# Kernel optimization log

Measured on AMD Instinct MI355X. Metric: run time of the kernel, lower is better.

## Reference

```python
import jax, jax.numpy as jnp
import numpy as np

T, HID, D, NQ, NKV = 4096, 2048, 128, 16, 4
THETA = 10000.0


def _rope(x, pos):
    # x: [T, N, D], non-interleaved (rotate_half) RoPE
    half = D // 2
    inv_freq = 1.0 / (THETA ** (jnp.arange(0, half, dtype=jnp.float32) / half))
    freqs = pos.astype(jnp.float32)[:, None] * inv_freq[None, :]  # [T, half]
    cos = jnp.cos(freqs)[:, None, :]  # [T, 1, half]
    sin = jnp.sin(freqs)[:, None, :]
    x1, x2 = x[..., :half], x[..., half:]
    return jnp.concatenate([x1 * cos - x2 * sin, x2 * cos + x1 * sin], axis=-1)


def setup_inputs() -> dict:
    key = jax.random.key(0)
    ks = jax.random.split(key, 5)
    s = 0.02
    return {
        "hidden_states": jax.random.normal(ks[0], (T, HID), jnp.float32),
        "wq": jax.random.normal(ks[1], (HID, HID), jnp.float32) * s,
        "wk": jax.random.normal(ks[2], (NKV * D, HID), jnp.float32) * s,
        "wv": jax.random.normal(ks[3], (NKV * D, HID), jnp.float32) * s,
        "wo": jax.random.normal(ks[4], (HID, HID), jnp.float32) * s,
        "position_ids": jnp.arange(T, dtype=jnp.int32),
    }


def reference(hidden_states, wq, wk, wv, wo, position_ids):
    q = (hidden_states @ wq.T).reshape(T, NQ, D)
    k = (hidden_states @ wk.T).reshape(T, NKV, D)
    v = (hidden_states @ wv.T).reshape(T, NKV, D)
    q = _rope(q, position_ids)
    k = _rope(k, position_ids)
    # GQA: share each KV head across NQ//NKV query heads
    rep = NQ // NKV
    k = jnp.repeat(k, rep, axis=1)  # [T, NQ, D]
    v = jnp.repeat(v, rep, axis=1)
    scale = 1.0 / jnp.sqrt(jnp.float32(D))
    scores = jnp.einsum("qhd,khd->hqk", q, k) * scale  # [NQ, T, T]
    causal = jnp.tril(jnp.ones((T, T), dtype=bool))
    scores = jnp.where(causal[None, :, :], scores, jnp.float32(-1e30))
    probs = jax.nn.softmax(scores, axis=-1)
    out = jnp.einsum("hqk,khd->qhd", probs, v).reshape(T, HID)
    return out @ wo.T
```

## Files before the change

kernel.cpp:

```cpp
#include <hip/hip_runtime.h>
#include <hip/hip_bf16.h>
#include <cstdint>

#define T_    4096
#define HID_  2048
#define DH    128
#define NQ_   16
#define NKV_  4
#define QKVW  3072

typedef __attribute__((ext_vector_type(8))) short bf16x8;
typedef __attribute__((ext_vector_type(4))) float f32x4;
typedef __attribute__((ext_vector_type(16))) float f32x16;
typedef __attribute__((ext_vector_type(4))) float f4;
typedef __attribute__((ext_vector_type(4))) short s4;

__device__ __forceinline__ short f2bf(float f) {
  union { float f; unsigned u; } x; x.f = f;
  unsigned r = x.u + 0x7fffu + ((x.u >> 16) & 1u);
  return (short)(r >> 16);
}
__device__ __forceinline__ float bf2f(short s) {
  return __uint_as_float(((unsigned)(unsigned short)s) << 16);
}
__device__ __forceinline__ unsigned pkbf2(float a, float b) {
  union { __hip_bfloat162 h; unsigned u; } c;
  c.h = __float22bfloat162_rn(make_float2(a, b));
  return c.u;
}

__device__ __forceinline__ void gload16(const void* g, void* l) {
  __builtin_amdgcn_global_load_lds(
      (const __attribute__((address_space(1))) unsigned*)g,
      (__attribute__((address_space(3))) unsigned*)l, 16, 0, 0);
}

#define MFMA16(a, b, c) __builtin_amdgcn_mfma_f32_16x16x32_bf16(a, b, c, 0, 0, 0)
#define MFMA32(a, b, c) __builtin_amdgcn_mfma_f32_32x32x16_bf16(a, b, c, 0, 0, 0)

#define Z16 {0.f,0.f,0.f,0.f,0.f,0.f,0.f,0.f,0.f,0.f,0.f,0.f,0.f,0.f,0.f,0.f}
#define SCL2 0.127517432f

#define C_HS 2097152u
#define C_WQ (C_HS + 1048576u)
#define C_WK (C_WQ + 262144u)
#define C_WV (C_WK + 262144u)
#define C_WO (C_WV + 1048576u)
__global__ void cvt_all(const float* __restrict__ hs, const float* __restrict__ wq,
                        const float* __restrict__ wk, const float* __restrict__ wv,
                        const float* __restrict__ wo, short* __restrict__ hs_bf,
                        short* __restrict__ w1_bf, short* __restrict__ wo_bf) {
  const unsigned stride = gridDim.x * blockDim.x;
  for (unsigned i = blockIdx.x * blockDim.x + threadIdx.x; i < C_WO; i += stride) {
    const float* s; short* d; unsigned off;
    if (i < C_HS)      { s = hs; d = hs_bf;           off = i; }
    else if (i < C_WQ) { s = wq; d = w1_bf;           off = i - C_HS; }
    else if (i < C_WK) { s = wk; d = w1_bf + 4194304; off = i - C_WQ; }
    else if (i < C_WV) { s = wv; d = w1_bf + 5242880; off = i - C_WK; }
    else               { s = wo; d = wo_bf;           off = i - C_WV; }
    f4 v = ((const f4*)s)[off];
    s4 o;
    o[0] = f2bf(v[0]); o[1] = f2bf(v[1]); o[2] = f2bf(v[2]); o[3] = f2bf(v[3]);
    ((s4*)d)[off] = o;
  }
}

template <int BF16OUT>
__global__ __launch_bounds__(256) void gemm_bt(const short* __restrict__ A,
                                               const short* __restrict__ B,
                                               void* __restrict__ Cp,
                                               int N, int K) {
  __shared__ short lA[128 * 32];
  __shared__ short lB[128 * 32];
  const int nb = gridDim.x * gridDim.y;
  const int lin = blockIdx.y * gridDim.x + blockIdx.x;
  const int per = nb >> 3;
  const int wg = (lin & 7) * per + (lin >> 3);
  const int bx = wg % gridDim.x;
  const int by = wg / gridDim.x;

  const int tid = threadIdx.x;
  const int lane = tid & 63;
  const int w = tid >> 6;
  const int wr = w >> 1, wc = w & 1;
  const int l15 = lane & 15, l4 = lane >> 4;
  f32x4 acc[4][4];
#pragma unroll
  for (int m = 0; m < 4; m++)
#pragma unroll
    for (int n = 0; n < 4; n++) acc[m][n] = f32x4{0.f, 0.f, 0.f, 0.f};

  const short* Ag = A + (size_t)bx * 128 * K;
  const short* Bg = B + (size_t)by * 128 * K;

  for (int kt = 0; kt < K; kt += 32) {
#pragma unroll
    for (int i = 0; i < 2; ++i) {
      const int cb = i * 256 + w * 64;
      const int c = cb + lane;
      const int row = c >> 2, eo = (c & 3) << 3;
      gload16(Ag + (size_t)row * K + kt + eo, &lA[cb * 8]);
      gload16(Bg + (size_t)row * K + kt + eo, &lB[cb * 8]);
    }
    __syncthreads();
    bf16x8 af[4], bfr[4];
#pragma unroll
    for (int m = 0; m < 4; m++)
      af[m] = *(const bf16x8*)&lA[(wr * 64 + m * 16 + l15) * 32 + l4 * 8];
#pragma unroll
    for (int n = 0; n < 4; n++)
      bfr[n] = *(const bf16x8*)&lB[(wc * 64 + n * 16 + l15) * 32 + l4 * 8];
#pragma unroll
    for (int m = 0; m < 4; m++)
#pragma unroll
      for (int n = 0; n < 4; n++)
        acc[m][n] = MFMA16(af[m], bfr[n], acc[m][n]);
    __syncthreads();
  }

  const int r0 = bx * 128 + wr * 64;
  const int c0 = by * 128 + wc * 64;
#pragma unroll
  for (int m = 0; m < 4; m++)
#pragma unroll
    for (int n = 0; n < 4; n++)
#pragma unroll
      for (int r = 0; r < 4; r++) {
        const int row = r0 + m * 16 + l4 * 4 + r;
        const int col = c0 + n * 16 + l15;
        if (BF16OUT)
          ((short*)Cp)[(size_t)row * N + col] = f2bf(acc[m][n][r]);
        else
          ((float*)Cp)[(size_t)row * N + col] = acc[m][n][r];
      }
}

__global__ void rope_k(short* __restrict__ qkv, const int* __restrict__ pos) {
  const int row = blockIdx.x;
  const int sub = threadIdx.x >> 6;
  const int d = threadIdx.x & 63;
  const int head = blockIdx.y * 4 + sub;
  const int col0 = (head < NQ_) ? head * DH : HID_ + (head - NQ_) * DH;
  const float scl = (head < NQ_) ? SCL2 : 1.0f;
  short* p = qkv + (size_t)row * QKVW + col0;
  const float fp = (float)pos[row];
  const float freq = fp * powf(10000.0f, -(float)d * (1.0f / 64.0f));
  const float sn = sinf(freq), cs = cosf(freq);
  const float x1 = bf2f(p[d]);
  const float x2 = bf2f(p[d + 64]);
  p[d] = f2bf((x1 * cs - x2 * sn) * scl);
  p[d + 64] = f2bf((x2 * cs + x1 * sn) * scl);
}


#define PRE(j)                                                                      \
  {                                                                                 \
    const int kv0e = (j) * 128, kv0o = (j) * 128 + 64;                              \
    _Pragma("unroll") for (int i = 0; i < 2; i++) {                                 \
      const int idx = i * 512 + tid;                                                \
      const int row = idx >> 4, e = (idx & 15) << 3;                                \
      kre[i] = *(const bf16x8*)(kbase + (size_t)(kv0e + row) * QKVW + e);           \
      kro[i] = *(const bf16x8*)(kbase + (size_t)(kv0o + row) * QKVW + e);           \
    }                                                                               \
    {                                                                               \
      const int rp = tid >> 4, e = (tid & 15) << 3;                                 \
      vre[0] = *(const bf16x8*)(vbase + (size_t)(kv0e + 2 * rp) * QKVW + e);        \
      vre[1] = *(const bf16x8*)(vbase + (size_t)(kv0e + 2 * rp + 1) * QKVW + e);    \
      vro[0] = *(const bf16x8*)(vbase + (size_t)(kv0o + 2 * rp) * QKVW + e);        \
      vro[1] = *(const bf16x8*)(vbase + (size_t)(kv0o + 2 * rp + 1) * QKVW + e);    \
    }                                                                               \
  }

#define WRITEBUF(bufp)                                                          \
  {                                                                             \
    char* sKe_ = (bufp);                                                        \
    char* sKo_ = (bufp) + 16384;                                                \
    char* sVe_ = (bufp) + 32768;                                                \
    char* sVo_ = (bufp) + 49152;                                                \
    _Pragma("unroll") for (int i = 0; i < 2; i++) {                             \
      const int idx = i * 512 + tid;                                            \
      const int row = idx >> 4, e16 = (idx & 15) << 4;                          \
      const int swz = (((row >> 3) ^ row) & 7) << 4;                            \
      *(bf16x8*)(sKe_ + row * 256 + (e16 ^ swz)) = kre[i];                      \
      *(bf16x8*)(sKo_ + row * 256 + (e16 ^ swz)) = kro[i];                      \
    }                                                                           \
    {                                                                           \
      const int rp = tid >> 4, e = (tid & 15) << 3;                             \
      const int rp2 = (rp & ~6) | ((rp & 2) << 1) | ((rp & 4) >> 1);            \
      _Pragma("unroll") for (int jj = 0; jj < 8; jj++) {                        \
        const int d = e + jj;                                                   \
        const int swz = (((d >> 3) ^ d) & 7) << 4;                              \
        const unsigned pe = ((unsigned)(unsigned short)vre[0][jj]) |            \
                            (((unsigned)(unsigned short)vre[1][jj]) << 16);     \
        const unsigned po = ((unsigned)(unsigned short)vro[0][jj]) |            \
                            (((unsigned)(unsigned short)vro[1][jj]) << 16);     \
        *(unsigned*)(sVe_ + d * 128 + ((rp2 * 4) ^ swz)) = pe;                  \
        *(unsigned*)(sVo_ + d * 128 + ((rp2 * 4) ^ swz)) = po;                  \
      }                                                                         \
    }                                                                           \
  }

__global__ __launch_bounds__(512) void attn_k(const short* __restrict__ qkv,
                                              short* __restrict__ aout) {
  __shared__ __align__(16) char smem[67584];
  float* ml = (float*)(smem + 65536);

  const int lin = blockIdx.x;
  const int xcd = lin & 7;
  const int slot = lin >> 3;
  const int kvh = xcd >> 1;
  const int qb = 127 - (slot * 2 + (xcd & 1));
  const int tid = threadIdx.x, lane = tid & 63, w = tid >> 6;
  const int head = w & 3, sp = w >> 2;
  const int hi = lane >> 5, l31 = lane & 31;
  const int h = kvh * 4 + head;

  const short* kbase = qkv + HID_ + kvh * DH;
  const short* vbase = qkv + HID_ + NKV_ * DH + kvh * DH;
  const int spoff = sp ? 16384 : 0;

  const int qrow0 = qb * 32;
  const int ntiles = qb / 2 + 1;
  const int nsuper = (ntiles + 1) >> 1;
  const int myq = qrow0 + l31;

  bf16x8 qf[8];
  {
    const short* qp = qkv + (size_t)myq * QKVW + h * DH + hi * 8;
#pragma unroll
    for (int c = 0; c < 8; c++) qf[c] = *(const bf16x8*)(qp + c * 16);
  }
  f32x16 o[4] = {Z16, Z16, Z16, Z16};
  float m = -3e38f, l = 0.f;

  bf16x8 kre[2], kro[2], vre[2], vro[2];
  PRE(0)

  for (int j = 0; j < nsuper; ++j) {
    __syncthreads();
    WRITEBUF(smem)
    __syncthreads();
    if (j + 1 < nsuper) PRE(j + 1)
    const char* bK = smem + spoff;
    const char* bV = smem + 32768 + spoff;

    const int t = 2 * j + sp;
    if (t < ntiles) {
      const int kv0 = t * 64;
      f32x16 s0 = Z16, s1 = Z16;
      const int sw0 = (((l31 >> 3) ^ l31) & 7) << 4;
      const int r1 = 32 + l31;
      const int sw1 = (((r1 >> 3) ^ r1) & 7) << 4;
      __builtin_amdgcn_s_setprio(1);
#pragma unroll
      for (int c = 0; c < 8; c++) {
        const int co = c * 32 + hi * 16;
        const bf16x8 k0 = *(const bf16x8*)(bK + l31 * 256 + (co ^ sw0));
        const bf16x8 k1 = *(const bf16x8*)(bK + r1 * 256 + (co ^ sw1));
        s0 = MFMA32(k0, qf[c], s0);
        s1 = MFMA32(k1, qf[c], s1);
      }
      __builtin_amdgcn_s_setprio(0);
      float sv0[16], sv1[16];
      if (t == ntiles - 1) {
#pragma unroll
        for (int r = 0; r < 16; r++) {
          const int kk = (r & 3) + 8 * (r >> 2) + 4 * hi;
          sv0[r] = (kv0 + kk <= myq) ? s0[r] : -1e30f;
          sv1[r] = (kv0 + 32 + kk <= myq) ? s1[r] : -1e30f;
        }
      } else {
#pragma unroll
        for (int r = 0; r < 16; r++) {
          sv0[r] = s0[r];
          sv1[r] = s1[r];
        }
      }
      float mx[8];
#pragma unroll
      for (int r = 0; r < 8; r++)
        mx[r] = fmaxf(fmaxf(sv0[r], sv0[r + 8]), fmaxf(sv1[r], sv1[r + 8]));
#pragma unroll
      for (int st = 4; st > 0; st >>= 1)
#pragma unroll
        for (int r = 0; r < 4; r++)
          if (r < st) mx[r] = fmaxf(mx[r], mx[r + st]);
      float pm = fmaxf(mx[0], __shfl_xor(mx[0], 32));
      if (__any(pm > m + 11.5f)) {
        const float mn = fmaxf(m, pm);
        const float al = exp2f(m - mn);
        m = mn;
        l *= al;
#pragma unroll
        for (int r = 0; r < 16; r++) {
          const float ar = __shfl(al, (r & 3) + 8 * (r >> 2) + 4 * hi);
#pragma unroll
          for (int dt = 0; dt < 4; dt++) o[dt][r] *= ar;
        }
      }
      float pv0[16], pv1[16];
#pragma unroll
      for (int r = 0; r < 16; r++) {
        pv0[r] = exp2f(sv0[r] - m);
        pv1[r] = exp2f(sv1[r] - m);
      }
      float sum[8];
#pragma unroll
      for (int r = 0; r < 8; r++)
        sum[r] = (pv0[r] + pv0[r + 8]) + (pv1[r] + pv1[r + 8]);
#pragma unroll
      for (int st = 4; st > 0; st >>= 1)
#pragma unroll
        for (int r = 0; r < 4; r++)
          if (r < st) sum[r] = sum[r] + sum[r + st];
      l += sum[0] + __shfl_xor(sum[0], 32);

      unsigned W0[8], W1[8];
#pragma unroll
      for (int i = 0; i < 8; i++) {
        W0[i] = pkbf2(pv0[2 * i], pv0[2 * i + 1]);
        W1[i] = pkbf2(pv1[2 * i], pv1[2 * i + 1]);
      }
#pragma unroll
      for (int kt = 0; kt < 2; kt++) {
#pragma unroll
        for (int hc = 0; hc < 2; hc++) {
          union { unsigned u[4]; bf16x8 v; } fr;
#pragma unroll
          for (int mm = 0; mm < 4; mm++)
            fr.u[mm] = kt ? W1[hc * 4 + mm] : W0[hc * 4 + mm];
          const int ko = kt * 64 + hc * 32 + hi * 16;
          __builtin_amdgcn_s_setprio(1);
#pragma unroll
          for (int dt = 0; dt < 4; dt++) {
            const int row = dt * 32 + l31;
            const int swz = (((row >> 3) ^ row) & 7) << 4;
            const bf16x8 vf = *(const bf16x8*)(bV + row * 128 + (ko ^ swz));
            o[dt] = MFMA32(fr.v, vf, o[dt]);
          }
          __builtin_amdgcn_s_setprio(0);
        }
      }
    }
  }

  if (lane < 32) {
    ml[((head * 2 + sp) * 2) * 32 + lane] = m;
    ml[((head * 2 + sp) * 2 + 1) * 32 + lane] = l;
  }
  __syncthreads();
  const float mo = ml[((head * 2 + (1 - sp)) * 2) * 32 + l31];
  const float lo = ml[((head * 2 + (1 - sp)) * 2 + 1) * 32 + l31];
  const float M = fmaxf(m, mo);
  const float aown = exp2f(m - M);
  const float ltot = l * aown + lo * exp2f(mo - M);
#pragma unroll
  for (int r = 0; r < 16; r++) {
    const float ar = __shfl(aown, (r & 3) + 8 * (r >> 2) + 4 * hi);
#pragma unroll
    for (int dt = 0; dt < 4; dt++) o[dt][r] *= ar;
  }
  float* Ob = (float*)smem + head * 4096;
  if (sp == 1) {
#pragma unroll
    for (int r = 0; r < 16; r++) {
      const int q = (r & 3) + 8 * (r >> 2) + 4 * hi;
#pragma unroll
      for (int dt = 0; dt < 4; dt++) Ob[q * 128 + dt * 32 + l31] = o[dt][r];
    }
  }
  __syncthreads();
  if (sp == 0) {
    const float ri = 1.0f / ltot;
#pragma unroll
    for (int r = 0; r < 16; r++) {
      const float rr = __shfl(ri, (r & 3) + 8 * (r >> 2) + 4 * hi);
      const int q = (r & 3) + 8 * (r >> 2) + 4 * hi;
#pragma unroll
      for (int dt = 0; dt < 4; dt++) {
        const float val = (o[dt][r] + Ob[q * 128 + dt * 32 + l31]) * rr;
        aout[(size_t)(qrow0 + q) * HID_ + h * DH + dt * 32 + l31] = f2bf(val);
      }
    }
  }
}

extern "C" void kernel_launch(void* const* d_in, const int* in_sizes, int n_in,
                              void* d_out, int out_size, void* d_ws, size_t ws_size,
                              hipStream_t stream) {
  const float* hs = (const float*)d_in[0];
  const float* wq = (const float*)d_in[1];
  const float* wk = (const float*)d_in[2];
  const float* wv = (const float*)d_in[3];
  const float* wo = (const float*)d_in[4];
  const int* pos = (const int*)d_in[5];
  float* out = (float*)d_out;

  const size_t SZ_HS = (size_t)T_ * HID_;
  const size_t SZ_WQ = (size_t)HID_ * HID_;
  const size_t SZ_W1 = (size_t)QKVW * HID_;
  const size_t SZ_QKV = (size_t)T_ * QKVW;

  short* hs_bf = (short*)d_ws;
  short* w1_bf = hs_bf + SZ_HS;
  short* wo_bf = w1_bf + SZ_W1;
  short* qkv = wo_bf + SZ_WQ;
  short* attn = qkv + SZ_QKV;

  cvt_all<<<2048, 256, 0, stream>>>(hs, wq, wk, wv, wo, hs_bf, w1_bf, wo_bf);

  gemm_bt<1><<<dim3(T_ / 128, QKVW / 128), 256, 0, stream>>>(hs_bf, w1_bf, qkv, QKVW, HID_);

  rope_k<<<dim3(T_, 5), 256, 0, stream>>>(qkv, pos);

  attn_k<<<dim3(512), 512, 0, stream>>>(qkv, attn);

  gemm_bt<0><<<dim3(T_ / 128, HID_ / 128), 256, 0, stream>>>(attn, wo_bf, out, HID_, HID_);
}
```

Baseline: 286.1 us.

## Double GEMM K-tile with XOR swizzle; load attention K tiles directly to LDS

The projection GEMM now stages a 64-wide K slice per iteration instead of 32, with an XOR-swizzled LDS layout to avoid bank conflicts. This halves the number of barrier pairs per tile and doubles the MFMAs issued between them. In the attention kernel, K tiles are now loaded with direct global-to-LDS loads (gload16) instead of going through registers. Only V is still prefetched into registers and transposed. Because the K load is now issued at the start of each iteration rather than prefetched one iteration ahead, K latency is exposed before the barrier. In exchange, register pressure drops.

```diff
diff --git a/kernel.cpp b/kernel.cpp
--- a/kernel.cpp
+++ b/kernel.cpp
@@ -70,8 +70,8 @@
                                                const short* __restrict__ B,
                                                void* __restrict__ Cp,
                                                int N, int K) {
-  __shared__ short lA[128 * 32];
-  __shared__ short lB[128 * 32];
+  __shared__ short lA[128 * 64];
+  __shared__ short lB[128 * 64];
   const int nb = gridDim.x * gridDim.y;
   const int lin = blockIdx.y * gridDim.x + blockIdx.x;
   const int per = nb >> 3;
@@ -93,28 +93,42 @@
   const short* Ag = A + (size_t)bx * 128 * K;
   const short* Bg = B + (size_t)by * 128 * K;
 
-  for (int kt = 0; kt < K; kt += 32) {
-#pragma unroll
-    for (int i = 0; i < 2; ++i) {
+  for (int kt = 0; kt < K; kt += 64) {
+#pragma unroll
+    for (int i = 0; i < 4; ++i) {
       const int cb = i * 256 + w * 64;
       const int c = cb + lane;
-      const int row = c >> 2, eo = (c & 3) << 3;
-      gload16(Ag + (size_t)row * K + kt + eo, &lA[cb * 8]);
-      gload16(Bg + (size_t)row * K + kt + eo, &lB[cb * 8]);
+      const int row = c >> 3;
+      const int x = (c & 7) << 4;
+      const int sx = x ^ ((row & 7) << 4);
+      gload16(Ag + (size_t)row * K + kt + (sx >> 1), (char*)lA + cb * 16);
+      gload16(Bg + (size_t)row * K + kt + (sx >> 1), (char*)lB + cb * 16);
     }
     __syncthreads();
-    bf16x8 af[4], bfr[4];
+    bf16x8 af[4][2], bfr[4][2];
+#pragma unroll
+    for (int m = 0; m < 4; m++) {
+      const int row = wr * 64 + m * 16 + l15;
+      const int sw = (row & 7) << 4;
+#pragma unroll
+      for (int kk = 0; kk < 2; kk++)
+        af[m][kk] = *(const bf16x8*)((const char*)lA + row * 128 + ((kk * 64 + l4 * 16) ^ sw));
+    }
+#pragma unroll
+    for (int n = 0; n < 4; n++) {
+      const int row = wc * 64 + n * 16 + l15;
+      const int sw = (row & 7) << 4;
+#pragma unroll
+      for (int kk = 0; kk < 2; kk++)
+        bfr[n][kk] = *(const bf16x8*)((const char*)lB + row * 128 + ((kk * 64 + l4 * 16) ^ sw));
+    }
 #pragma unroll
     for (int m = 0; m < 4; m++)
-      af[m] = *(const bf16x8*)&lA[(wr * 64 + m * 16 + l15) * 32 + l4 * 8];
-#pragma unroll
-    for (int n = 0; n < 4; n++)
-      bfr[n] = *(const bf16x8*)&lB[(wc * 64 + n * 16 + l15) * 32 + l4 * 8];
-#pragma unroll
-    for (int m = 0; m < 4; m++)
-#pragma unroll
-      for (int n = 0; n < 4; n++)
-        acc[m][n] = MFMA16(af[m], bfr[n], acc[m][n]);
+#pragma unroll
+      for (int n = 0; n < 4; n++) {
+        acc[m][n] = MFMA16(af[m][0], bfr[n][0], acc[m][n]);
+        acc[m][n] = MFMA16(af[m][1], bfr[n][1], acc[m][n]);
+      }
     __syncthreads();
   }
 
@@ -153,50 +167,45 @@
 }
 
 
-#define PRE(j)                                                                      \
+#define PREV(j)                                                                     \
+  {                                                                                 \
+    const int kv0e = (j) * 128, kv0o = (j) * 128 + 64;                              \
+    const int rp = tid >> 4, e = (tid & 15) << 3;                                   \
+    vre[0] = *(const bf16x8*)(vbase + (size_t)(kv0e + 2 * rp) * QKVW + e);          \
+    vre[1] = *(const bf16x8*)(vbase + (size_t)(kv0e + 2 * rp + 1) * QKVW + e);      \
+    vro[0] = *(const bf16x8*)(vbase + (size_t)(kv0o + 2 * rp) * QKVW + e);          \
+    vro[1] = *(const bf16x8*)(vbase + (size_t)(kv0o + 2 * rp + 1) * QKVW + e);      \
+  }
+
+#define KGLDS(j)                                                                    \
   {                                                                                 \
     const int kv0e = (j) * 128, kv0o = (j) * 128 + 64;                              \
     _Pragma("unroll") for (int i = 0; i < 2; i++) {                                 \
-      const int idx = i * 512 + tid;                                                \
-      const int row = idx >> 4, e = (idx & 15) << 3;                                \
-      kre[i] = *(const bf16x8*)(kbase + (size_t)(kv0e + row) * QKVW + e);           \
-      kro[i] = *(const bf16x8*)(kbase + (size_t)(kv0o + row) * QKVW + e);           \
+      const int cb = i * 512 + w * 64;                 \
+      const int c = cb + lane;                                                      \
+      const int row = c >> 4;                         \
+      const int x = (c & 15) << 4;                                                  \
+      const int sx = x ^ ((((row >> 3) ^ row) & 7) << 4);                           \
+      gload16(kbase + (size_t)(kv0e + row) * QKVW + (sx >> 1), sKe + cb * 16);      \
+      gload16(kbase + (size_t)(kv0o + row) * QKVW + (sx >> 1), sKo + cb * 16);      \
     }                                                                               \
-    {                                                                               \
-      const int rp = tid >> 4, e = (tid & 15) << 3;                                 \
-      vre[0] = *(const bf16x8*)(vbase + (size_t)(kv0e + 2 * rp) * QKVW + e);        \
-      vre[1] = *(const bf16x8*)(vbase + (size_t)(kv0e + 2 * rp + 1) * QKVW + e);    \
-      vro[0] = *(const bf16x8*)(vbase + (size_t)(kv0o + 2 * rp) * QKVW + e);        \
-      vro[1] = *(const bf16x8*)(vbase + (size_t)(kv0o + 2 * rp + 1) * QKVW + e);    \
-    }                                                                               \
-  }
-
-#define WRITEBUF(bufp)                                                          \
+  }
+
+#define WRITEV()                                                                \
   {                                                                             \
-    char* sKe_ = (bufp);                                                        \
-    char* sKo_ = (bufp) + 16384;                                                \
-    char* sVe_ = (bufp) + 32768;                                                \
-    char* sVo_ = (bufp) + 49152;                                                \
-    _Pragma("unroll") for (int i = 0; i < 2; i++) {                             \
-      const int idx = i * 512 + tid;                                            \
-      const int row = idx >> 4, e16 = (idx & 15) << 4;                          \
-      const int swz = (((row >> 3) ^ row) & 7) << 4;                            \
-      *(bf16x8*)(sKe_ + row * 256 + (e16 ^ swz)) = kre[i];                      \
-      *(bf16x8*)(sKo_ + row * 256 + (e16 ^ swz)) = kro[i];                      \
-    }                                                                           \
-    {                                                                           \
-      const int rp = tid >> 4, e = (tid & 15) << 3;                             \
-      const int rp2 = (rp & ~6) | ((rp & 2) << 1) | ((rp & 4) >> 1);            \
-      _Pragma("unroll") for (int jj = 0; jj < 8; jj++) {                        \
-        const int d = e + jj;                                                   \
-        const int swz = (((d >> 3) ^ d) & 7) << 4;                              \
-        const unsigned pe = ((unsigned)(unsigned short)vre[0][jj]) |            \
-                            (((unsigned)(unsigned short)vre[1][jj]) << 16);     \
-        const unsigned po = ((unsigned)(unsigned short)vro[0][jj]) |            \
-                            (((unsigned)(unsigned short)vro[1][jj]) << 16);     \
-        *(unsigned*)(sVe_ + d * 128 + ((rp2 * 4) ^ swz)) = pe;                  \
-        *(unsigned*)(sVo_ + d * 128 + ((rp2 * 4) ^ swz)) = po;                  \
-      }                                                                         \
+    char* sVe_ = smem + 32768;                                                  \
+    char* sVo_ = smem + 49152;                                                  \
+    const int rp = tid >> 4, e = (tid & 15) << 3;                               \
+    const int rp2 = (rp & ~6) | ((rp & 2) << 1) | ((rp & 4) >> 1);              \
+    _Pragma("unroll") for (int jj = 0; jj < 8; jj++) {                          \
+      const int d = e + jj;                                                     \
+      const int swz = (((d >> 3) ^ d) & 7) << 4;                                \
+      const unsigned pe = ((unsigned)(unsigned short)vre[0][jj]) |              \
+                          (((unsigned)(unsigned short)vre[1][jj]) << 16);       \
+      const unsigned po = ((unsigned)(unsigned short)vro[0][jj]) |              \
+                          (((unsigned)(unsigned short)vro[1][jj]) << 16);       \
+      *(unsigned*)(sVe_ + d * 128 + ((rp2 * 4) ^ swz)) = pe;                    \
+      *(unsigned*)(sVo_ + d * 128 + ((rp2 * 4) ^ swz)) = po;                    \
     }                                                                           \
   }
 
@@ -204,6 +213,8 @@
                                               short* __restrict__ aout) {
   __shared__ __align__(16) char smem[67584];
   float* ml = (float*)(smem + 65536);
+  char* sKe = smem;
+  char* sKo = smem + 16384;
 
   const int lin = blockIdx.x;
   const int xcd = lin & 7;
@@ -233,14 +244,15 @@
   f32x16 o[4] = {Z16, Z16, Z16, Z16};
   float m = -3e38f, l = 0.f;
 
-  bf16x8 kre[2], kro[2], vre[2], vro[2];
-  PRE(0)
+  bf16x8 vre[2], vro[2];
+  PREV(0)
 
   for (int j = 0; j < nsuper; ++j) {
     __syncthreads();
-    WRITEBUF(smem)
+    KGLDS(j)
+    WRITEV()
     __syncthreads();
-    if (j + 1 < nsuper) PRE(j + 1)
+    if (j + 1 < nsuper) PREV(j + 1)
     const char* bK = smem + spoff;
     const char* bV = smem + 32768 + spoff;
 
```

Result: faster. 278.0 us (-2.8%).

## Double GEMM K-tile with XOR-swizzled LDS and vectorize RoPE with shared sin/cos

Applied to the files above, without the earlier changes.

The GEMM K-step goes from 32 to 64 and the LDS layout gets an XOR swizzle. This halves the barrier and loop overhead per unit of work and is meant to avoid LDS bank conflicts on fragment reads. The RoPE kernel now handles one token row per block with 320 threads. It computes cos/sin once into shared memory and processes 4 elements per thread with vector loads and stores, which cuts repeated transcendental evaluation and narrow memory accesses. LDS use in the GEMM doubles, which may reduce occupancy.

```diff
diff --git a/kernel.cpp b/kernel.cpp
--- a/kernel.cpp
+++ b/kernel.cpp
@@ -70,8 +70,8 @@
                                                const short* __restrict__ B,
                                                void* __restrict__ Cp,
                                                int N, int K) {
-  __shared__ short lA[128 * 32];
-  __shared__ short lB[128 * 32];
+  __shared__ short lA[128 * 64];
+  __shared__ short lB[128 * 64];
   const int nb = gridDim.x * gridDim.y;
   const int lin = blockIdx.y * gridDim.x + blockIdx.x;
   const int per = nb >> 3;
@@ -93,28 +93,42 @@
   const short* Ag = A + (size_t)bx * 128 * K;
   const short* Bg = B + (size_t)by * 128 * K;
 
-  for (int kt = 0; kt < K; kt += 32) {
-#pragma unroll
-    for (int i = 0; i < 2; ++i) {
+  for (int kt = 0; kt < K; kt += 64) {
+#pragma unroll
+    for (int i = 0; i < 4; ++i) {
       const int cb = i * 256 + w * 64;
       const int c = cb + lane;
-      const int row = c >> 2, eo = (c & 3) << 3;
-      gload16(Ag + (size_t)row * K + kt + eo, &lA[cb * 8]);
-      gload16(Bg + (size_t)row * K + kt + eo, &lB[cb * 8]);
+      const int row = c >> 3;
+      const int x = (c & 7) << 4;
+      const int sx = x ^ ((row & 7) << 4);
+      gload16(Ag + (size_t)row * K + kt + (sx >> 1), (char*)lA + cb * 16);
+      gload16(Bg + (size_t)row * K + kt + (sx >> 1), (char*)lB + cb * 16);
     }
     __syncthreads();
-    bf16x8 af[4], bfr[4];
+    bf16x8 af[4][2], bfr[4][2];
+#pragma unroll
+    for (int m = 0; m < 4; m++) {
+      const int row = wr * 64 + m * 16 + l15;
+      const int sw = (row & 7) << 4;
+#pragma unroll
+      for (int kk = 0; kk < 2; kk++)
+        af[m][kk] = *(const bf16x8*)((const char*)lA + row * 128 + ((kk * 64 + l4 * 16) ^ sw));
+    }
+#pragma unroll
+    for (int n = 0; n < 4; n++) {
+      const int row = wc * 64 + n * 16 + l15;
+      const int sw = (row & 7) << 4;
+#pragma unroll
+      for (int kk = 0; kk < 2; kk++)
+        bfr[n][kk] = *(const bf16x8*)((const char*)lB + row * 128 + ((kk * 64 + l4 * 16) ^ sw));
+    }
 #pragma unroll
     for (int m = 0; m < 4; m++)
-      af[m] = *(const bf16x8*)&lA[(wr * 64 + m * 16 + l15) * 32 + l4 * 8];
-#pragma unroll
-    for (int n = 0; n < 4; n++)
-      bfr[n] = *(const bf16x8*)&lB[(wc * 64 + n * 16 + l15) * 32 + l4 * 8];
-#pragma unroll
-    for (int m = 0; m < 4; m++)
-#pragma unroll
-      for (int n = 0; n < 4; n++)
-        acc[m][n] = MFMA16(af[m], bfr[n], acc[m][n]);
+#pragma unroll
+      for (int n = 0; n < 4; n++) {
+        acc[m][n] = MFMA16(af[m][0], bfr[n][0], acc[m][n]);
+        acc[m][n] = MFMA16(af[m][1], bfr[n][1], acc[m][n]);
+      }
     __syncthreads();
   }
 
@@ -136,22 +150,35 @@
 }
 
 __global__ void rope_k(short* __restrict__ qkv, const int* __restrict__ pos) {
+  __shared__ float cs[64], sn[64];
   const int row = blockIdx.x;
-  const int sub = threadIdx.x >> 6;
-  const int d = threadIdx.x & 63;
-  const int head = blockIdx.y * 4 + sub;
+  const int tid = threadIdx.x;
+  if (tid < 64) {
+    const float fp = (float)pos[row];
+    const float freq = fp * powf(10000.0f, -(float)tid * (1.0f / 64.0f));
+    cs[tid] = cosf(freq);
+    sn[tid] = sinf(freq);
+  }
+  __syncthreads();
+  const int p = tid * 4;
+  const int head = p >> 6;
+  const int d0 = p & 63;
   const int col0 = (head < NQ_) ? head * DH : HID_ + (head - NQ_) * DH;
   const float scl = (head < NQ_) ? SCL2 : 1.0f;
-  short* p = qkv + (size_t)row * QKVW + col0;
-  const float fp = (float)pos[row];
-  const float freq = fp * powf(10000.0f, -(float)d * (1.0f / 64.0f));
-  const float sn = sinf(freq), cs = cosf(freq);
-  const float x1 = bf2f(p[d]);
-  const float x2 = bf2f(p[d + 64]);
-  p[d] = f2bf((x1 * cs - x2 * sn) * scl);
-  p[d + 64] = f2bf((x2 * cs + x1 * sn) * scl);
-}
-
+  short* q = qkv + (size_t)row * QKVW + col0 + d0;
+  s4 x1 = *(const s4*)q;
+  s4 x2 = *(const s4*)(q + 64);
+  s4 o1, o2;
+#pragma unroll
+  for (int j = 0; j < 4; j++) {
+    const float c = cs[d0 + j], s = sn[d0 + j];
+    const float a = bf2f(x1[j]), b = bf2f(x2[j]);
+    o1[j] = f2bf((a * c - b * s) * scl);
+    o2[j] = f2bf((b * c + a * s) * scl);
+  }
+  *(s4*)q = o1;
+  *(s4*)(q + 64) = o2;
+}
 
 #define PRE(j)                                                                      \
   {                                                                                 \
@@ -411,7 +438,7 @@
 
   gemm_bt<1><<<dim3(T_ / 128, QKVW / 128), 256, 0, stream>>>(hs_bf, w1_bf, qkv, QKVW, HID_);
 
-  rope_k<<<dim3(T_, 5), 256, 0, stream>>>(qkv, pos);
+  rope_k<<<dim3(T_), 320, 0, stream>>>(qkv, pos);
 
   attn_k<<<dim3(512), 512, 0, stream>>>(qkv, attn);
 
```

After: 256.1 us. 10.5% less time.
